# Kernel tuning notes

Hardware: AMD Instinct MI355X
Metric: run time of the kernel (lower is better)

The kernel has to match this reference:

```python
import jax, jax.numpy as jnp
import numpy as np
import math

N_EMBD = 1024
N_HEAD = 16
HEAD_DIM = N_EMBD // N_HEAD

def setup_inputs() -> dict:
    key = jax.random.key(0)
    k1, k2, k3, k4, k5 = jax.random.split(key, 5)
    s = 1.0 / math.sqrt(N_EMBD)
    x = jax.random.normal(k1, (4, 2048, N_EMBD), dtype=jnp.float32)
    W_qkv = jax.random.normal(k2, (N_EMBD, 3 * N_EMBD), dtype=jnp.float32) * s
    b_qkv = jnp.zeros((3 * N_EMBD,), dtype=jnp.float32)
    W_proj = jax.random.normal(k3, (N_EMBD, N_EMBD), dtype=jnp.float32) * s
    b_proj = jnp.zeros((N_EMBD,), dtype=jnp.float32)
    return {"x": x, "W_qkv": W_qkv, "b_qkv": b_qkv, "W_proj": W_proj, "b_proj": b_proj}

def reference(x, W_qkv, b_qkv, W_proj, b_proj):
    B, T, C = x.shape
    H, D = N_HEAD, HEAD_DIM
    qkv = x @ W_qkv + b_qkv                      # (B,T,3C)
    qkv = qkv.reshape(B, T, 3, H, D)
    q = jnp.transpose(qkv[:, :, 0], (0, 2, 1, 3))  # (B,H,T,D)
    k = jnp.transpose(qkv[:, :, 1], (0, 2, 1, 3))
    v = jnp.transpose(qkv[:, :, 2], (0, 2, 1, 3))
    scale = 1.0 / math.sqrt(D)
    att = jnp.einsum('bhtd,bhsd->bhts', q, k) * scale  # (B,H,T,T)
    causal = jnp.tril(jnp.ones((T, T), dtype=bool))
    att = jnp.where(causal[None, None], att, -jnp.inf)
    att = jax.nn.softmax(att, axis=-1)
    out = jnp.einsum('bhts,bhsd->bhtd', att, v)   # (B,H,T,D)
    out = jnp.transpose(out, (0, 2, 1, 3)).reshape(B, T, C)
    return out @ W_proj + b_proj
```

## Files before the change

kernel.cpp:

```cpp
#include <hip/hip_runtime.h>
#include <stdint.h>


typedef __attribute__((ext_vector_type(8))) __bf16 bf16x8_t;
typedef __attribute__((ext_vector_type(4))) float f32x4_t;
typedef __attribute__((ext_vector_type(16))) float f32x16_t;
typedef __attribute__((ext_vector_type(4))) unsigned short u16x4_t;
typedef __attribute__((ext_vector_type(4))) unsigned int u32x4_t;

static __device__ __forceinline__ unsigned short f2bf(float f) {
  union { float f; unsigned u; } c; c.f = f;
  unsigned r = c.u + 0x7FFFu + ((c.u >> 16) & 1u);
  return (unsigned short)(r >> 16);
}

static __device__ __forceinline__ unsigned cvt_pk_bf16(float lo, float hi) {
  unsigned r;
  asm volatile("v_cvt_pk_bf16_f32 %0, %1, %2" : "=v"(r) : "v"(lo), "v"(hi));
  return r;
}

static __device__ __forceinline__ void perm32swap(unsigned& a, unsigned& b) {
  asm volatile("v_permlane32_swap_b32 %0, %1" : "+v"(a), "+v"(b));
}

static __device__ __forceinline__ f32x16_t zero16() {
  f32x16_t v;
#pragma unroll
  for (int i = 0; i < 16; ++i) v[i] = 0.f;
  return v;
}

static __device__ __forceinline__ void gload16(const void* g, void* lds) {
  __builtin_amdgcn_global_load_lds(
      (const __attribute__((address_space(1))) unsigned int*)g,
      (__attribute__((address_space(3))) unsigned int*)(uint32_t)(uintptr_t)lds,
      16, 0, 0);
}

__global__ __launch_bounds__(256) void k_cast_bf16(const float* __restrict__ in,
                                                   unsigned short* __restrict__ out) {
  int i = blockIdx.x * 256 + threadIdx.x;
  float4 v = ((const float4*)in)[i];
  u16x4_t r = { f2bf(v.x), f2bf(v.y), f2bf(v.z), f2bf(v.w) };
  ((u16x4_t*)out)[i] = r;
}

__global__ __launch_bounds__(256) void k_transpose_cast(const float* __restrict__ W,
                                                        unsigned short* __restrict__ Wt,
                                                        int Kd, int Nd) {
  __shared__ float tile[32][33];
  int n0 = blockIdx.x * 32, k0 = blockIdx.y * 32;
  int tx = threadIdx.x, ty = threadIdx.y;
#pragma unroll
  for (int i = 0; i < 4; ++i)
    tile[ty + 8 * i][tx] = W[(size_t)(k0 + ty + 8 * i) * Nd + n0 + tx];
  __syncthreads();
#pragma unroll
  for (int i = 0; i < 4; ++i)
    Wt[(size_t)(n0 + ty + 8 * i) * Kd + k0 + tx] = f2bf(tile[tx][ty + 8 * i]);
}

static __device__ __forceinline__ void gemm_core(
    const unsigned short* __restrict__ A, const unsigned short* __restrict__ Bt,
    int Kd, int bm0, int bn0,
    unsigned short (*As)[128 * 64], unsigned short (*Bs)[256 * 64],
    f32x4_t acc[4][4]) {
  const int tid = threadIdx.x;
  const int lane = tid & 63;
  const int wid = tid >> 6;
  const int wm = wid >> 2, wn = wid & 3;
  const int l15 = lane & 15, lhi = lane >> 4;
  const int trow = tid >> 3;
  const int schunk = ((tid & 7) ^ (trow & 7)) * 8;
  const unsigned short* aS = A + (size_t)(bm0 + trow) * Kd + schunk;
  const unsigned short* bS = Bt + (size_t)(bn0 + trow) * Kd + schunk;
  const int NK = Kd >> 6;

  auto STAGE = [&](int kt, int sl) {
    const size_t ko = (size_t)kt * 64;
#pragma unroll
    for (int j = 0; j < 2; ++j)
      gload16(aS + ko + (size_t)(64 * j) * Kd, &As[sl][j * 4096 + tid * 8]);
#pragma unroll
    for (int j = 0; j < 4; ++j)
      gload16(bS + ko + (size_t)(64 * j) * Kd, &Bs[sl][j * 4096 + tid * 8]);
  };

  STAGE(0, 0);
  asm volatile("s_waitcnt vmcnt(0)" ::: "memory");
  __builtin_amdgcn_s_barrier();
  __builtin_amdgcn_sched_barrier(0);
  for (int kt = 0; kt < NK; ++kt) {
    const int sl = kt & 1;
    if (kt + 1 < NK) STAGE(kt + 1, sl ^ 1);
    __builtin_amdgcn_sched_barrier(0);
#pragma unroll
    for (int ks = 0; ks < 2; ++ks) {
      const int ch = ((4 * ks + lhi) ^ (l15 & 7)) * 8;
      bf16x8_t af[4], bfr[4];
#pragma unroll
      for (int m = 0; m < 4; ++m)
        af[m] = *(const bf16x8_t*)&As[sl][(wm * 64 + m * 16 + l15) * 64 + ch];
#pragma unroll
      for (int n = 0; n < 4; ++n)
        bfr[n] = *(const bf16x8_t*)&Bs[sl][(wn * 64 + n * 16 + l15) * 64 + ch];
#pragma unroll
      for (int m = 0; m < 4; ++m)
#pragma unroll
        for (int n = 0; n < 4; ++n)
          acc[m][n] = __builtin_amdgcn_mfma_f32_16x16x32_bf16(af[m], bfr[n], acc[m][n], 0, 0, 0);
    }
    asm volatile("s_waitcnt vmcnt(0)" ::: "memory");
    __builtin_amdgcn_s_barrier();
    __builtin_amdgcn_sched_barrier(0);
  }
}

__global__ __launch_bounds__(512, 2) void k_gemm_qkv(
    const unsigned short* __restrict__ A, const unsigned short* __restrict__ Bt,
    const float* __restrict__ bias,
    unsigned short* __restrict__ Qo, unsigned short* __restrict__ Ko,
    unsigned short* __restrict__ Vo) {
  __shared__ alignas(16) unsigned short As[2][128 * 64];
  __shared__ alignas(16) unsigned short Bs[2][256 * 64];
  const int orig = blockIdx.x;
  const int swz = (orig & 7) * 96 + (orig >> 3);
  const int by = swz / 12, bx = swz % 12;
  f32x4_t acc[4][4];
  f32x4_t z = {0.f, 0.f, 0.f, 0.f};
#pragma unroll
  for (int m = 0; m < 4; ++m)
#pragma unroll
    for (int n = 0; n < 4; ++n) acc[m][n] = z;
  gemm_core(A, Bt, 1024, by * 128, bx * 256, As, Bs, acc);
  const int tid = threadIdx.x, lane = tid & 63;
  const int wid = tid >> 6, wm = wid >> 2, wn = wid & 3;
  const int l15 = lane & 15, lhi = lane >> 4;
#pragma unroll
  for (int n = 0; n < 4; ++n) {
    int col = bx * 256 + wn * 64 + n * 16 + l15;
    int which = col >> 10;
    int h = (col >> 6) & 15;
    int d = col & 63;
    float bv = bias[col];
#pragma unroll
    for (int m = 0; m < 4; ++m)
#pragma unroll
      for (int r = 0; r < 4; ++r) {
        int row = by * 128 + wm * 64 + m * 16 + lhi * 4 + r;
        int b = row >> 11, t = row & 2047;
        float val = acc[m][n][r] + bv;
        if (which == 0)
          Qo[(size_t)((b * 16 + h) * 2048 + t) * 64 + d] = f2bf(val * 0.18033688011112042f);
        else if (which == 1)
          Ko[(size_t)((b * 16 + h) * 2048 + t) * 64 + d] = f2bf(val);
        else
          Vo[(size_t)((b * 16 + h) * 64 + d) * 2048 + t] = f2bf(val);
      }
  }
}

__global__ __launch_bounds__(512, 2) void k_gemm_proj(
    const unsigned short* __restrict__ A, const unsigned short* __restrict__ Bt,
    const float* __restrict__ bias, float* __restrict__ out) {
  __shared__ alignas(16) unsigned short As[2][128 * 64];
  __shared__ alignas(16) unsigned short Bs[2][256 * 64];
  const int orig = blockIdx.x;
  const int swz = (orig & 7) * 32 + (orig >> 3);
  const int by = swz >> 2, bx = swz & 3;
  f32x4_t acc[4][4];
  f32x4_t z = {0.f, 0.f, 0.f, 0.f};
#pragma unroll
  for (int m = 0; m < 4; ++m)
#pragma unroll
    for (int n = 0; n < 4; ++n) acc[m][n] = z;
  gemm_core(A, Bt, 1024, by * 128, bx * 256, As, Bs, acc);
  const int tid = threadIdx.x, lane = tid & 63;
  const int wid = tid >> 6, wm = wid >> 2, wn = wid & 3;
  const int l15 = lane & 15, lhi = lane >> 4;
#pragma unroll
  for (int n = 0; n < 4; ++n) {
    int col = bx * 256 + wn * 64 + n * 16 + l15;
    float bv = bias[col];
#pragma unroll
    for (int m = 0; m < 4; ++m)
#pragma unroll
      for (int r = 0; r < 4; ++r) {
        int row = by * 128 + wm * 64 + m * 16 + lhi * 4 + r;
        out[(size_t)row * 1024 + col] = acc[m][n][r] + bv;
      }
  }
}

__global__ __launch_bounds__(256) void k_attn(const unsigned short* __restrict__ Q,
                                              const unsigned short* __restrict__ K,
                                              const unsigned short* __restrict__ Vt,
                                              unsigned short* __restrict__ O) {
  __shared__ alignas(16) unsigned short KT[2][4096];
  __shared__ alignas(16) unsigned short VT[2][4096];
  const int flat = blockIdx.x;
  const int bx = 15 - (flat >> 6);
  const int bh = flat & 63;
  const int tid = threadIdx.x;
  const int lane = tid & 63;
  const int w = tid >> 6;
  const int l31 = lane & 31;
  const int hi = lane >> 5;
  const int sw = l31 & 7;
  const unsigned short* Qh = Q + (size_t)bh * 2048 * 64;
  const unsigned short* Kh = K + (size_t)bh * 2048 * 64;
  const unsigned short* Vh = Vt + (size_t)bh * 64 * 2048;
  const int qrow = bx * 128 + w * 32;
  const int qg = qrow + l31;
  const int NT = 2 * bx + 2;

  bf16x8_t qf[4];
#pragma unroll
  for (int s = 0; s < 4; ++s)
    qf[s] = *(const bf16x8_t*)&Qh[(size_t)qg * 64 + s * 16 + hi * 8];

  f32x16_t ot0 = zero16(), ot1 = zero16();
  float m_r = -1e30f, l_r = 0.f;

  const int srow = tid >> 3;
  const int ssw = 8 * ((tid & 7) ^ (srow & 7));
  auto STAGE = [&](int t_, int buf_) {
#pragma unroll
    for (int i = 0; i < 2; ++i) {
      const int r_ = i * 32 + srow;
      gload16(Kh + (size_t)(t_ * 64 + r_) * 64 + ssw, &KT[buf_][i * 2048 + tid * 8]);
      gload16(Vh + (size_t)r_ * 2048 + t_ * 64 + ssw, &VT[buf_][i * 2048 + tid * 8]);
    }
  };

  STAGE(0, 0);
  __syncthreads();
  for (int t = 0; t < NT; ++t) {
    const int buf = t & 1;
    if (t + 1 < NT) STAGE(t + 1, buf ^ 1);
    if (t * 64 <= qrow + 31) {
      f32x16_t st[2];
#pragma unroll
      for (int tt = 0; tt < 2; ++tt) {
        st[tt] = zero16();
        const unsigned short* kr = &KT[buf][(tt * 32 + l31) * 64];
#pragma unroll
        for (int s = 0; s < 4; ++s) {
          bf16x8_t kf = *(const bf16x8_t*)&kr[((2 * s + hi) ^ sw) * 8];
          st[tt] = __builtin_amdgcn_mfma_f32_32x32x16_bf16(kf, qf[s], st[tt], 0, 0, 0);
        }
      }
      if (t * 64 + 63 > qrow) {
#pragma unroll
        for (int tt = 0; tt < 2; ++tt)
#pragma unroll
          for (int r = 0; r < 16; ++r) {
            int kv = t * 64 + tt * 32 + (r & 3) + 8 * (r >> 2) + 4 * hi;
            if (kv > qg) st[tt][r] = -1e30f;
          }
      }
      float mx = st[0][0];
#pragma unroll
      for (int tt = 0; tt < 2; ++tt)
#pragma unroll
        for (int r = 0; r < 16; ++r) mx = fmaxf(mx, st[tt][r]);
      mx = fmaxf(mx, __shfl_xor(mx, 32));
      float mnew = fmaxf(m_r, mx);
      float resc = __builtin_amdgcn_exp2f(m_r - mnew);
      float u = 0.f;
#pragma unroll
      for (int tt = 0; tt < 2; ++tt)
#pragma unroll
        for (int r = 0; r < 16; ++r) {
          float pv = __builtin_amdgcn_exp2f(st[tt][r] - mnew);
          st[tt][r] = pv;
          u += pv;
        }
      u += __shfl_xor(u, 32);
      l_r = l_r * resc + u;
      m_r = mnew;
      ot0 *= resc;
      ot1 *= resc;
#pragma unroll
      for (int tt = 0; tt < 2; ++tt) {
        unsigned W0 = cvt_pk_bf16(st[tt][0], st[tt][1]);
        unsigned W1 = cvt_pk_bf16(st[tt][2], st[tt][3]);
        unsigned W2 = cvt_pk_bf16(st[tt][4], st[tt][5]);
        unsigned W3 = cvt_pk_bf16(st[tt][6], st[tt][7]);
        unsigned W4 = cvt_pk_bf16(st[tt][8], st[tt][9]);
        unsigned W5 = cvt_pk_bf16(st[tt][10], st[tt][11]);
        unsigned W6 = cvt_pk_bf16(st[tt][12], st[tt][13]);
        unsigned W7 = cvt_pk_bf16(st[tt][14], st[tt][15]);
        perm32swap(W0, W2);
        perm32swap(W1, W3);
        perm32swap(W4, W6);
        perm32swap(W5, W7);
        u32x4_t fe = {W0, W1, W2, W3};
        u32x4_t fo = {W4, W5, W6, W7};
        bf16x8_t pe = __builtin_bit_cast(bf16x8_t, fe);
        bf16x8_t po = __builtin_bit_cast(bf16x8_t, fo);
        const unsigned short* vr0 = &VT[buf][l31 * 64];
        const unsigned short* vr1 = &VT[buf][(32 + l31) * 64];
        bf16x8_t ve0 = *(const bf16x8_t*)&vr0[((4 * tt + hi) ^ sw) * 8];
        bf16x8_t vo0 = *(const bf16x8_t*)&vr0[((4 * tt + 2 + hi) ^ sw) * 8];
        bf16x8_t ve1 = *(const bf16x8_t*)&vr1[((4 * tt + hi) ^ sw) * 8];
        bf16x8_t vo1 = *(const bf16x8_t*)&vr1[((4 * tt + 2 + hi) ^ sw) * 8];
        ot0 = __builtin_amdgcn_mfma_f32_32x32x16_bf16(ve0, pe, ot0, 0, 0, 0);
        ot0 = __builtin_amdgcn_mfma_f32_32x32x16_bf16(vo0, po, ot0, 0, 0, 0);
        ot1 = __builtin_amdgcn_mfma_f32_32x32x16_bf16(ve1, pe, ot1, 0, 0, 0);
        ot1 = __builtin_amdgcn_mfma_f32_32x32x16_bf16(vo1, po, ot1, 0, 0, 0);
      }
    }
    __syncthreads();
  }
  const float inv = 1.0f / l_r;
  const int b = bh >> 4, h = bh & 15;
  unsigned short* orow = O + (size_t)(b * 2048 + qg) * 1024 + h * 64;
#pragma unroll
  for (int m = 0; m < 4; ++m) {
    u16x4_t r0, r1;
#pragma unroll
    for (int j = 0; j < 4; ++j) {
      r0[j] = f2bf(ot0[4 * m + j] * inv);
      r1[j] = f2bf(ot1[4 * m + j] * inv);
    }
    *(u16x4_t*)&orow[8 * m + 4 * hi] = r0;
    *(u16x4_t*)&orow[32 + 8 * m + 4 * hi] = r1;
  }
}

extern "C" void kernel_launch(void* const* d_in, const int* in_sizes, int n_in,
                              void* d_out, int out_size, void* d_ws, size_t ws_size,
                              hipStream_t stream) {
  const float* x     = (const float*)d_in[0];
  const float* Wqkv  = (const float*)d_in[1];
  const float* bqkv  = (const float*)d_in[2];
  const float* Wproj = (const float*)d_in[3];
  const float* bproj = (const float*)d_in[4];
  float* out = (float*)d_out;

  char* ws = (char*)d_ws;
  unsigned short* xb     = (unsigned short*)(ws);
  unsigned short* wqkvT  = (unsigned short*)(ws + 16777216);
  unsigned short* wprojT = (unsigned short*)(ws + 23068672);
  unsigned short* Qb     = (unsigned short*)(ws + 25165824);
  unsigned short* Kb     = (unsigned short*)(ws + 41943040);
  unsigned short* Vb     = (unsigned short*)(ws + 58720256);
  unsigned short* Ob     = (unsigned short*)(ws + 75497472);

  k_cast_bf16<<<8192, 256, 0, stream>>>(x, xb);
  k_transpose_cast<<<dim3(96, 32), dim3(32, 8), 0, stream>>>(Wqkv, wqkvT, 1024, 3072);
  k_transpose_cast<<<dim3(32, 32), dim3(32, 8), 0, stream>>>(Wproj, wprojT, 1024, 1024);
  k_gemm_qkv<<<768, 512, 0, stream>>>(xb, wqkvT, bqkv, Qb, Kb, Vb);
  k_attn<<<1024, 256, 0, stream>>>(Qb, Kb, Vb, Ob);
  k_gemm_proj<<<256, 512, 0, stream>>>(Ob, wprojT, bproj, out);
}
```

Measured before the change: 271.4 us.

## Enlarge GEMM tiles to 256x256 with half-K LDS pipelining

The shared GEMM core now computes 256x256 output tiles, giving each wave 8x4 MFMA accumulators instead of 4x4, so more math is done per loaded byte. Each 64-wide K step is split into two 32-wide halves with their own swizzled LDS buffers. Loads for the next half are issued behind a partial vmcnt wait, and the MFMA block is wrapped in s_setprio. The intent is to raise arithmetic intensity and overlap global loads with compute. The cost is fewer blocks (384 for QKV, 128 for proj on a 256-CU part), roughly 128 KB of LDS per block, and much higher register pressure, all of which may hurt occupancy and load balance.

```diff
diff --git a/kernel.cpp b/kernel.cpp
--- a/kernel.cpp
+++ b/kernel.cpp
@@ -64,56 +64,65 @@
 static __device__ __forceinline__ void gemm_core(
     const unsigned short* __restrict__ A, const unsigned short* __restrict__ Bt,
     int Kd, int bm0, int bn0,
-    unsigned short (*As)[128 * 64], unsigned short (*Bs)[256 * 64],
-    f32x4_t acc[4][4]) {
+    unsigned short (*As)[8192], unsigned short (*Bs)[8192],
+    f32x4_t acc[8][4]) {
   const int tid = threadIdx.x;
   const int lane = tid & 63;
   const int wid = tid >> 6;
   const int wm = wid >> 2, wn = wid & 3;
-  const int l15 = lane & 15, lhi = lane >> 4;
-  const int trow = tid >> 3;
-  const int schunk = ((tid & 7) ^ (trow & 7)) * 8;
-  const unsigned short* aS = A + (size_t)(bm0 + trow) * Kd + schunk;
-  const unsigned short* bS = Bt + (size_t)(bn0 + trow) * Kd + schunk;
+  const int l15 = lane & 15, lhi = (lane >> 4) & 3;
+  const int r0 = tid >> 2;
+  const int cd = tid & 3;
   const int NK = Kd >> 6;
 
-  auto STAGE = [&](int kt, int sl) {
-    const size_t ko = (size_t)kt * 64;
-#pragma unroll
-    for (int j = 0; j < 2; ++j)
-      gload16(aS + ko + (size_t)(64 * j) * Kd, &As[sl][j * 4096 + tid * 8]);
-#pragma unroll
-    for (int j = 0; j < 4; ++j)
-      gload16(bS + ko + (size_t)(64 * j) * Kd, &Bs[sl][j * 4096 + tid * 8]);
+  auto STAGE = [&](int kt, int h, int sl) {
+#pragma unroll
+    for (int j = 0; j < 2; ++j) {
+      const int row = r0 + 128 * j;
+      const int sc = cd ^ ((row >> 1) & 3);
+      gload16(A + (size_t)(bm0 + row) * Kd + kt * 64 + h * 32 + sc * 8,
+              &As[sl * 2 + h][row * 32 + cd * 8]);
+    }
+#pragma unroll
+    for (int j = 0; j < 2; ++j) {
+      const int row = r0 + 128 * j;
+      const int sc = cd ^ ((row >> 1) & 3);
+      gload16(Bt + (size_t)(bn0 + row) * Kd + kt * 64 + h * 32 + sc * 8,
+              &Bs[sl * 2 + h][row * 32 + cd * 8]);
+    }
   };
 
-  STAGE(0, 0);
-  asm volatile("s_waitcnt vmcnt(0)" ::: "memory");
-  __builtin_amdgcn_s_barrier();
-  __builtin_amdgcn_sched_barrier(0);
+  STAGE(0, 0, 0);
+  STAGE(0, 1, 0);
   for (int kt = 0; kt < NK; ++kt) {
     const int sl = kt & 1;
-    if (kt + 1 < NK) STAGE(kt + 1, sl ^ 1);
-    __builtin_amdgcn_sched_barrier(0);
-#pragma unroll
-    for (int ks = 0; ks < 2; ++ks) {
-      const int ch = ((4 * ks + lhi) ^ (l15 & 7)) * 8;
-      bf16x8_t af[4], bfr[4];
-#pragma unroll
-      for (int m = 0; m < 4; ++m)
-        af[m] = *(const bf16x8_t*)&As[sl][(wm * 64 + m * 16 + l15) * 64 + ch];
-#pragma unroll
-      for (int n = 0; n < 4; ++n)
-        bfr[n] = *(const bf16x8_t*)&Bs[sl][(wn * 64 + n * 16 + l15) * 64 + ch];
-#pragma unroll
-      for (int m = 0; m < 4; ++m)
+    const int ktn = (kt + 1 < NK) ? kt + 1 : kt;
+#pragma unroll
+    for (int h = 0; h < 2; ++h) {
+      asm volatile("s_waitcnt vmcnt(4)" ::: "memory");
+      __builtin_amdgcn_sched_barrier(0);
+      __builtin_amdgcn_s_barrier();
+      __builtin_amdgcn_sched_barrier(0);
+      STAGE(ktn, h, sl ^ 1);
+      bf16x8_t af[8], bfr[4];
+#pragma unroll
+      for (int m = 0; m < 8; ++m) {
+        const int ar = wm * 128 + m * 16 + l15;
+        af[m] = *(const bf16x8_t*)&As[sl * 2 + h][ar * 32 + ((lhi ^ ((ar >> 1) & 3)) << 3)];
+      }
+#pragma unroll
+      for (int n = 0; n < 4; ++n) {
+        const int br = wn * 64 + n * 16 + l15;
+        bfr[n] = *(const bf16x8_t*)&Bs[sl * 2 + h][br * 32 + ((lhi ^ ((br >> 1) & 3)) << 3)];
+      }
+      __builtin_amdgcn_s_setprio(1);
+#pragma unroll
+      for (int m = 0; m < 8; ++m)
 #pragma unroll
         for (int n = 0; n < 4; ++n)
           acc[m][n] = __builtin_amdgcn_mfma_f32_16x16x32_bf16(af[m], bfr[n], acc[m][n], 0, 0, 0);
-    }
-    asm volatile("s_waitcnt vmcnt(0)" ::: "memory");
-    __builtin_amdgcn_s_barrier();
-    __builtin_amdgcn_sched_barrier(0);
+      __builtin_amdgcn_s_setprio(0);
+    }
   }
 }
 
@@ -122,21 +131,21 @@
     const float* __restrict__ bias,
     unsigned short* __restrict__ Qo, unsigned short* __restrict__ Ko,
     unsigned short* __restrict__ Vo) {
-  __shared__ alignas(16) unsigned short As[2][128 * 64];
-  __shared__ alignas(16) unsigned short Bs[2][256 * 64];
+  __shared__ alignas(16) unsigned short As[4][8192];
+  __shared__ alignas(16) unsigned short Bs[4][8192];
   const int orig = blockIdx.x;
-  const int swz = (orig & 7) * 96 + (orig >> 3);
+  const int swz = (orig & 7) * 48 + (orig >> 3);
   const int by = swz / 12, bx = swz % 12;
-  f32x4_t acc[4][4];
+  f32x4_t acc[8][4];
   f32x4_t z = {0.f, 0.f, 0.f, 0.f};
 #pragma unroll
-  for (int m = 0; m < 4; ++m)
+  for (int m = 0; m < 8; ++m)
 #pragma unroll
     for (int n = 0; n < 4; ++n) acc[m][n] = z;
-  gemm_core(A, Bt, 1024, by * 128, bx * 256, As, Bs, acc);
+  gemm_core(A, Bt, 1024, by * 256, bx * 256, As, Bs, acc);
   const int tid = threadIdx.x, lane = tid & 63;
   const int wid = tid >> 6, wm = wid >> 2, wn = wid & 3;
-  const int l15 = lane & 15, lhi = lane >> 4;
+  const int l15 = lane & 15, lhi = (lane >> 4) & 3;
 #pragma unroll
   for (int n = 0; n < 4; ++n) {
     int col = bx * 256 + wn * 64 + n * 16 + l15;
@@ -145,10 +154,10 @@
     int d = col & 63;
     float bv = bias[col];
 #pragma unroll
-    for (int m = 0; m < 4; ++m)
+    for (int m = 0; m < 8; ++m)
 #pragma unroll
       for (int r = 0; r < 4; ++r) {
-        int row = by * 128 + wm * 64 + m * 16 + lhi * 4 + r;
+        int row = by * 256 + wm * 128 + m * 16 + lhi * 4 + r;
         int b = row >> 11, t = row & 2047;
         float val = acc[m][n][r] + bv;
         if (which == 0)
@@ -164,30 +173,30 @@
 __global__ __launch_bounds__(512, 2) void k_gemm_proj(
     const unsigned short* __restrict__ A, const unsigned short* __restrict__ Bt,
     const float* __restrict__ bias, float* __restrict__ out) {
-  __shared__ alignas(16) unsigned short As[2][128 * 64];
-  __shared__ alignas(16) unsigned short Bs[2][256 * 64];
+  __shared__ alignas(16) unsigned short As[4][8192];
+  __shared__ alignas(16) unsigned short Bs[4][8192];
   const int orig = blockIdx.x;
-  const int swz = (orig & 7) * 32 + (orig >> 3);
+  const int swz = (orig & 7) * 16 + (orig >> 3);
   const int by = swz >> 2, bx = swz & 3;
-  f32x4_t acc[4][4];
+  f32x4_t acc[8][4];
   f32x4_t z = {0.f, 0.f, 0.f, 0.f};
 #pragma unroll
-  for (int m = 0; m < 4; ++m)
+  for (int m = 0; m < 8; ++m)
 #pragma unroll
     for (int n = 0; n < 4; ++n) acc[m][n] = z;
-  gemm_core(A, Bt, 1024, by * 128, bx * 256, As, Bs, acc);
+  gemm_core(A, Bt, 1024, by * 256, bx * 256, As, Bs, acc);
   const int tid = threadIdx.x, lane = tid & 63;
   const int wid = tid >> 6, wm = wid >> 2, wn = wid & 3;
-  const int l15 = lane & 15, lhi = lane >> 4;
+  const int l15 = lane & 15, lhi = (lane >> 4) & 3;
 #pragma unroll
   for (int n = 0; n < 4; ++n) {
     int col = bx * 256 + wn * 64 + n * 16 + l15;
     float bv = bias[col];
 #pragma unroll
-    for (int m = 0; m < 4; ++m)
+    for (int m = 0; m < 8; ++m)
 #pragma unroll
       for (int r = 0; r < 4; ++r) {
-        int row = by * 128 + wm * 64 + m * 16 + lhi * 4 + r;
+        int row = by * 256 + wm * 128 + m * 16 + lhi * 4 + r;
         out[(size_t)row * 1024 + col] = acc[m][n][r] + bv;
       }
   }
@@ -352,7 +361,7 @@
   k_cast_bf16<<<8192, 256, 0, stream>>>(x, xb);
   k_transpose_cast<<<dim3(96, 32), dim3(32, 8), 0, stream>>>(Wqkv, wqkvT, 1024, 3072);
   k_transpose_cast<<<dim3(32, 32), dim3(32, 8), 0, stream>>>(Wproj, wprojT, 1024, 1024);
-  k_gemm_qkv<<<768, 512, 0, stream>>>(xb, wqkvT, bqkv, Qb, Kb, Vb);
+  k_gemm_qkv<<<384, 512, 0, stream>>>(xb, wqkvT, bqkv, Qb, Kb, Vb);
   k_attn<<<1024, 256, 0, stream>>>(Qb, Kb, Vb, Ob);
-  k_gemm_proj<<<256, 512, 0, stream>>>(Ob, wprojT, bproj, out);
-}
+  k_gemm_proj<<<128, 512, 0, stream>>>(Ob, wprojT, bproj, out);
+}
```

Result: slower. 290.9 us (+7.2%).
